# Kernel optimization log

Hardware: AMD Instinct MI355X
Metric: run time of the kernel (lower is better)

## Reference

```python
import jax, jax.numpy as jnp
import numpy as np

# ---- init_kwargs-derived constants ----
B, IN_F, OUT_F = 8192, 4096, 4096
W_SCALE = 0.01          # layer_params['w_scale']
B_SCALE = 0.01          # layer_params['b_scale']
IN_MIN, IN_MAX = -1.0, 1.0   # input_stats
NUM_BITS = 8
QMAX = 2 ** NUM_BITS - 1
IN_SCALE = (IN_MAX - IN_MIN) / QMAX
IN_ZP = int(round(-IN_MIN / (IN_SCALE + 1e-12)))


def setup_inputs() -> dict:
    key = jax.random.key(0)
    k1, k2, k3 = jax.random.split(key, 3)
    x_float = jax.random.normal(k1, (B, IN_F), dtype=jnp.float32)
    # int8-range weights/bias (stored as int32 containers)
    w_q = jax.random.randint(k2, (OUT_F, IN_F), -128, 128, dtype=jnp.int32)
    b_q = jax.random.randint(k3, (OUT_F,), -128, 128, dtype=jnp.int32)
    return {"x_float": x_float, "w_q": w_q, "b_q": b_q}


def reference(x_float, w_q, b_q):
    # quantize input to uint8 range [0,255]
    x_q = jnp.clip(jnp.round(x_float / IN_SCALE + IN_ZP), 0, 255).astype(jnp.int32)
    x_shifted = x_q - IN_ZP                       # [B, IN_F] int32
    # exact int32 accumulation matmul: [B, IN_F] @ [IN_F, OUT_F]
    acc_int = jnp.matmul(x_shifted, w_q.T, preferred_element_type=jnp.int32)
    out = acc_int.astype(jnp.float32) * (IN_SCALE * W_SCALE)
    out = out + b_q.astype(jnp.float32) * B_SCALE  # bias_float = b_q * b_scale
    return out
```

## Files before the change

### kernel.cpp

```cpp
#include <hip/hip_runtime.h>
#include <stdint.h>

constexpr int Mdim = 8192;
constexpr int Ndim = 4096;
constexpr int Kdim = 4096;
constexpr int NT = Kdim / 128;

#define ISF        ((float)(2.0 / 255.0))
#define OUT_SCALE  ((float)(2.0 / 255.0 * 0.01))
#define BSCALE     0.01f

typedef int i32x4 __attribute__((ext_vector_type(4)));

__global__ __launch_bounds__(256) void quantize_x(const float* __restrict__ x,
                                                  int* __restrict__ x8,
                                                  int ngroups) {
  int idx = blockIdx.x * 256 + threadIdx.x;
  int stride = gridDim.x * 256;
  for (int g = idx; g < ngroups; g += stride) {
    float4 v = reinterpret_cast<const float4*>(x)[g];
    int a0 = (int)rintf(v.x / ISF + 127.0f);
    int a1 = (int)rintf(v.y / ISF + 127.0f);
    int a2 = (int)rintf(v.z / ISF + 127.0f);
    int a3 = (int)rintf(v.w / ISF + 127.0f);
    a0 = a0 < 0 ? 0 : (a0 > 255 ? 255 : a0); a0 -= 128;
    a1 = a1 < 0 ? 0 : (a1 > 255 ? 255 : a1); a1 -= 128;
    a2 = a2 < 0 ? 0 : (a2 > 255 ? 255 : a2); a2 -= 128;
    a3 = a3 < 0 ? 0 : (a3 > 255 ? 255 : a3); a3 -= 128;
    x8[g] = (a0 & 0xff) | ((a1 & 0xff) << 8) | ((a2 & 0xff) << 16) |
            (int)(((unsigned)(a3 & 0xff)) << 24);
  }
}

__global__ __launch_bounds__(256) void convert_w(const int* __restrict__ wq,
                                                 int* __restrict__ w8,
                                                 int* __restrict__ wsum) {
  int row = blockIdx.x;
  const int4* src = reinterpret_cast<const int4*>(wq + (size_t)row * Kdim);
  int* dst = w8 + (size_t)row * (Kdim / 4);
  int s = 0;
#pragma unroll
  for (int i = 0; i < 4; ++i) {
    int idx = i * 256 + threadIdx.x;
    int4 v = src[idx];
    s += v.x + v.y + v.z + v.w;
    dst[idx] = (v.x & 0xff) | ((v.y & 0xff) << 8) | ((v.z & 0xff) << 16) |
               (int)(((unsigned)(v.w & 0xff)) << 24);
  }
  __shared__ int red[256];
  red[threadIdx.x] = s;
  __syncthreads();
  for (int off = 128; off; off >>= 1) {
    if ((int)threadIdx.x < off) red[threadIdx.x] += red[threadIdx.x + off];
    __syncthreads();
  }
  if (threadIdx.x == 0) wsum[row] = red[0];
}

#define AS1C const __attribute__((address_space(1))) void*
#define AS3  __attribute__((address_space(3))) void*
#define GLL(src, dst) __builtin_amdgcn_global_load_lds((AS1C)(src), (AS3)(dst), 16, 0, 0)
#define BAR() asm volatile("s_barrier" ::: "memory")
#define LGK0() do { asm volatile("s_waitcnt lgkmcnt(0)" ::: "memory"); \
                    __builtin_amdgcn_sched_barrier(0); } while (0)
#define VMC(N) asm volatile("s_waitcnt vmcnt(" #N ")" ::: "memory")
#define MFMA(a, b, c) __builtin_amdgcn_mfma_i32_16x16x64_i8(a, b, c, 0, 0, 0)
#define BBASE 98304

__global__ __launch_bounds__(512, 2) void gemm_i8_q(const int8_t* __restrict__ A8,
                                                    const int8_t* __restrict__ B8,
                                                    const int* __restrict__ wsum,
                                                    const int* __restrict__ bq,
                                                    float* __restrict__ out) {
  __shared__ uint8_t lds[163840];

  int bid = blockIdx.x;
  int wg = (bid & 7) * 64 + (bid >> 3);
  int bm = wg >> 4;
  int bn = wg & 15;

  const int tid = threadIdx.x;
  const int lane = tid & 63;
  const int wv = tid >> 6;
  const int wr = wv >> 2;
  const int wc = wv & 3;
  const int l15 = lane & 15, hi = lane >> 4;

  const int r3 = lane >> 3, s3 = lane & 7;
  const int swcol = (s3 ^ r3) << 4;
  const size_t aoff = (size_t)(bm * 256 + wv * 8 + r3) * Kdim + swcol;
  const size_t boff = (size_t)(bn * 256 + wv * 8 + r3) * Kdim + swcol;
  const int ldsw = wv * 1024;

#define ISSUE_A(P, t, half) do { \
    GLL(A8 + aoff + (size_t)(t) * 128 + (size_t)((half) * 128) * Kdim, \
        &lds[(P) * 32768 + (half) * 16384 + ldsw]); \
    GLL(A8 + aoff + (size_t)(t) * 128 + (size_t)((half) * 128 + 64) * Kdim, \
        &lds[(P) * 32768 + (half) * 16384 + 8192 + ldsw]); \
  } while (0)
#define ISSUE_B(P, t, half) do { \
    GLL(B8 + boff + (size_t)(t) * 128 + (size_t)((half) * 128) * Kdim, \
        &lds[BBASE + (P) * 32768 + (half) * 16384 + ldsw]); \
    GLL(B8 + boff + (size_t)(t) * 128 + (size_t)((half) * 128 + 64) * Kdim, \
        &lds[BBASE + (P) * 32768 + (half) * 16384 + 8192 + ldsw]); \
  } while (0)

  const int aRow = (wr * 128 + l15) * 128;
  const int bRow = (wc * 64 + l15) * 128;
  const int sl0 = (hi ^ (l15 & 7)) << 4;
  const int sl1 = ((4 + hi) ^ (l15 & 7)) << 4;

#define LDA(P, i, ks) (*reinterpret_cast<const i32x4*>( \
    &lds[(P) * 32768 + aRow + (i) * 2048 + ((ks) ? sl1 : sl0)]))
#define LDB(P, j, ks) (*reinterpret_cast<const i32x4*>( \
    &lds[BBASE + (P) * 32768 + bRow + (j) * 2048 + ((ks) ? sl1 : sl0)]))

  i32x4 acc[8][4];
#pragma unroll
  for (int i = 0; i < 8; ++i)
#pragma unroll
    for (int j = 0; j < 4; ++j) acc[i][j] = (i32x4){0, 0, 0, 0};

  ISSUE_A(0, 0, 0); ISSUE_A(0, 0, 1);
  ISSUE_B(0, 0, 0); ISSUE_B(0, 0, 1);
  ISSUE_A(1, 1, 0); ISSUE_A(1, 1, 1);
  VMC(4);
  BAR();

#define TILE(TA, TB, TA2, t, DOB, DOA, VM4, VM0) do { \
    i32x4 a_[4], B0[4], B1[4]; \
     \
    if (DOB) ISSUE_B((TB) ^ 1, (t) + 1, 0); \
    B0[0] = LDB(TB, 0, 0); B0[1] = LDB(TB, 1, 0); B0[2] = LDB(TB, 2, 0); B0[3] = LDB(TB, 3, 0); \
    a_[0] = LDA(TA, 0, 0); a_[1] = LDA(TA, 1, 0); a_[2] = LDA(TA, 2, 0); a_[3] = LDA(TA, 3, 0); \
    BAR(); LGK0(); __builtin_amdgcn_s_setprio(1); \
    _Pragma("unroll") for (int i = 0; i < 4; ++i) \
      _Pragma("unroll") for (int j = 0; j < 4; ++j) \
        acc[i][j] = MFMA(a_[i], B0[j], acc[i][j]); \
    __builtin_amdgcn_s_setprio(0); BAR(); \
     \
    if (DOB) ISSUE_B((TB) ^ 1, (t) + 1, 1); \
    a_[0] = LDA(TA, 4, 0); a_[1] = LDA(TA, 5, 0); a_[2] = LDA(TA, 6, 0); a_[3] = LDA(TA, 7, 0); \
    BAR(); LGK0(); __builtin_amdgcn_s_setprio(1); \
    _Pragma("unroll") for (int i = 0; i < 4; ++i) \
      _Pragma("unroll") for (int j = 0; j < 4; ++j) \
        acc[i + 4][j] = MFMA(a_[i], B0[j], acc[i + 4][j]); \
    __builtin_amdgcn_s_setprio(0); BAR(); \
     \
    if (DOA) ISSUE_A(TA2, (t) + 2, 0); \
    B1[0] = LDB(TB, 0, 1); B1[1] = LDB(TB, 1, 1); B1[2] = LDB(TB, 2, 1); B1[3] = LDB(TB, 3, 1); \
    a_[0] = LDA(TA, 0, 1); a_[1] = LDA(TA, 1, 1); a_[2] = LDA(TA, 2, 1); a_[3] = LDA(TA, 3, 1); \
    BAR(); LGK0(); __builtin_amdgcn_s_setprio(1); \
    _Pragma("unroll") for (int i = 0; i < 4; ++i) \
      _Pragma("unroll") for (int j = 0; j < 4; ++j) \
        acc[i][j] = MFMA(a_[i], B1[j], acc[i][j]); \
    __builtin_amdgcn_s_setprio(0); BAR(); \
     \
    if (DOA) ISSUE_A(TA2, (t) + 2, 1); \
    a_[0] = LDA(TA, 4, 1); a_[1] = LDA(TA, 5, 1); a_[2] = LDA(TA, 6, 1); a_[3] = LDA(TA, 7, 1); \
    BAR(); LGK0(); __builtin_amdgcn_s_setprio(1); \
    _Pragma("unroll") for (int i = 0; i < 4; ++i) \
      _Pragma("unroll") for (int j = 0; j < 4; ++j) \
        acc[i + 4][j] = MFMA(a_[i], B1[j], acc[i + 4][j]); \
    __builtin_amdgcn_s_setprio(0); \
    if (VM4) VMC(4); \
    if (VM0) VMC(0); \
    BAR(); \
  } while (0)

  for (int it = 0; it < 5; ++it) {
    int t = it * 6;
    TILE(0, 0, 2, t + 0, 1, 1, 1, 0);
    TILE(1, 1, 0, t + 1, 1, 1, 1, 0);
    TILE(2, 0, 1, t + 2, 1, 1, 1, 0);
    TILE(0, 1, 2, t + 3, 1, 1, 1, 0);
    TILE(1, 0, 0, t + 4, 1, 1, 1, 0);
    TILE(2, 1, 1, t + 5, 1, 1, 1, 0);
  }
  TILE(0, 0, 2, 30, 1, 0, 0, 1);
  TILE(1, 1, 0, 31, 0, 0, 0, 0);

#pragma unroll
  for (int j = 0; j < 4; ++j) {
    int col = bn * 256 + wc * 64 + j * 16 + l15;
    float fb = (float)bq[col] * BSCALE;
    int ws = wsum[col];
#pragma unroll
    for (int i = 0; i < 8; ++i) {
      int rbase = bm * 256 + wr * 128 + i * 16 + hi * 4;
#pragma unroll
      for (int p = 0; p < 4; ++p)
        out[(size_t)(rbase + p) * Ndim + col] = (float)(acc[i][j][p] + ws) * OUT_SCALE + fb;
    }
  }
#undef TILE
#undef ISSUE_A
#undef ISSUE_B
#undef LDA
#undef LDB
}

__global__ void fallback_kernel(const float* __restrict__ x, const int* __restrict__ wq,
                                const int* __restrict__ bq, float* __restrict__ out) {
  int col = blockIdx.x * 16 + (threadIdx.x & 15);
  int row = blockIdx.y * 16 + (threadIdx.x >> 4);
  const float* xr = x + (size_t)row * Kdim;
  const int* wr_ = wq + (size_t)col * Kdim;
  int acc = 0;
  for (int k = 0; k < Kdim; ++k) {
    int v = (int)rintf(xr[k] / ISF + 127.0f);
    v = v < 0 ? 0 : (v > 255 ? 255 : v);
    acc += (v - 127) * wr_[k];
  }
  out[(size_t)row * Ndim + col] = (float)acc * OUT_SCALE + (float)bq[col] * BSCALE;
}

extern "C" void kernel_launch(void* const* d_in, const int* in_sizes, int n_in,
                              void* d_out, int out_size, void* d_ws, size_t ws_size,
                              hipStream_t stream) {
  const float* x = (const float*)d_in[0];
  const int* wq = (const int*)d_in[1];
  const int* bq = (const int*)d_in[2];
  float* out = (float*)d_out;

  const size_t x8_bytes = (size_t)Mdim * Kdim;
  const size_t w8_bytes = (size_t)Ndim * Kdim;
  const size_t ws_need = x8_bytes + w8_bytes + (size_t)Ndim * sizeof(int);

  if (ws_size >= ws_need) {
    int8_t* x8 = (int8_t*)d_ws;
    int8_t* w8 = x8 + x8_bytes;
    int* wsum = (int*)(w8 + w8_bytes);

    quantize_x<<<2048, 256, 0, stream>>>(x, (int*)x8, Mdim * Kdim / 4);
    convert_w<<<Ndim, 256, 0, stream>>>(wq, (int*)w8, wsum);
    gemm_i8_q<<<(Mdim / 256) * (Ndim / 256), 512, 0, stream>>>(x8, w8, wsum, bq, out);
  } else {
    dim3 grid(Ndim / 16, Mdim / 16);
    fallback_kernel<<<grid, 256, 0, stream>>>(x, wq, bq, out);
  }
}
```

Baseline: 182.0 us.

## Software-pipeline LDS reads with partial lgkmcnt waits and fewer barriers

Restructures the per-tile schedule of the int8 GEMM. All global-to-LDS prefetches for the next tiles are issued at the start of each tile, and LDS fragment reads for later MFMA groups are issued ahead of the current group. Partial lgkmcnt waits replace the full waits and three of the four intra-tile s_barriers, so LDS latency overlaps with MFMA work. This raises register pressure (more live fragments) and relies on vmcnt/lgkmcnt counting being correct now that each tile has fewer barriers; issuing all prefetches early could race on LDS buffers if the triple-buffering is off.

```diff
diff --git a/kernel.cpp b/kernel.cpp
--- a/kernel.cpp
+++ b/kernel.cpp
@@ -61,17 +61,17 @@
 #define AS3  __attribute__((address_space(3))) void*
 #define GLL(src, dst) __builtin_amdgcn_global_load_lds((AS1C)(src), (AS3)(dst), 16, 0, 0)
 #define BAR() asm volatile("s_barrier" ::: "memory")
-#define LGK0() do { asm volatile("s_waitcnt lgkmcnt(0)" ::: "memory"); \
-                    __builtin_amdgcn_sched_barrier(0); } while (0)
+#define SB0() __builtin_amdgcn_sched_barrier(0)
+#define LGK(N) do { asm volatile("s_waitcnt lgkmcnt(" #N ")" ::: "memory"); SB0(); } while (0)
 #define VMC(N) asm volatile("s_waitcnt vmcnt(" #N ")" ::: "memory")
 #define MFMA(a, b, c) __builtin_amdgcn_mfma_i32_16x16x64_i8(a, b, c, 0, 0, 0)
 #define BBASE 98304
 
-__global__ __launch_bounds__(512, 2) void gemm_i8_q(const int8_t* __restrict__ A8,
-                                                    const int8_t* __restrict__ B8,
-                                                    const int* __restrict__ wsum,
-                                                    const int* __restrict__ bq,
-                                                    float* __restrict__ out) {
+__global__ __launch_bounds__(512, 2) void gemm_i8_pipe(const int8_t* __restrict__ A8,
+                                                       const int8_t* __restrict__ B8,
+                                                       const int* __restrict__ wsum,
+                                                       const int* __restrict__ bq,
+                                                       float* __restrict__ out) {
   __shared__ uint8_t lds[163840];
 
   int bid = blockIdx.x;
@@ -121,6 +121,12 @@
 #pragma unroll
     for (int j = 0; j < 4; ++j) acc[i][j] = (i32x4){0, 0, 0, 0};
 
+#define GRP(AV, BV, IOFF) do { \
+    _Pragma("unroll") for (int i = 0; i < 4; ++i) \
+      _Pragma("unroll") for (int j = 0; j < 4; ++j) \
+        acc[i + (IOFF)][j] = MFMA(AV[i], BV[j], acc[i + (IOFF)][j]); \
+  } while (0)
+
   ISSUE_A(0, 0, 0); ISSUE_A(0, 0, 1);
   ISSUE_B(0, 0, 0); ISSUE_B(0, 0, 1);
   ISSUE_A(1, 1, 0); ISSUE_A(1, 1, 1);
@@ -128,40 +134,38 @@
   BAR();
 
 #define TILE(TA, TB, TA2, t, DOB, DOA, VM4, VM0) do { \
-    i32x4 a_[4], B0[4], B1[4]; \
-     \
-    if (DOB) ISSUE_B((TB) ^ 1, (t) + 1, 0); \
+    if (DOB) { ISSUE_B((TB) ^ 1, (t) + 1, 0); ISSUE_B((TB) ^ 1, (t) + 1, 1); } \
+    if (DOA) { ISSUE_A(TA2, (t) + 2, 0); ISSUE_A(TA2, (t) + 2, 1); } \
+    i32x4 B0[4], B1[4], a0[4], a1[4], a2[4], a3[4]; \
+     \
     B0[0] = LDB(TB, 0, 0); B0[1] = LDB(TB, 1, 0); B0[2] = LDB(TB, 2, 0); B0[3] = LDB(TB, 3, 0); \
-    a_[0] = LDA(TA, 0, 0); a_[1] = LDA(TA, 1, 0); a_[2] = LDA(TA, 2, 0); a_[3] = LDA(TA, 3, 0); \
-    BAR(); LGK0(); __builtin_amdgcn_s_setprio(1); \
-    _Pragma("unroll") for (int i = 0; i < 4; ++i) \
-      _Pragma("unroll") for (int j = 0; j < 4; ++j) \
-        acc[i][j] = MFMA(a_[i], B0[j], acc[i][j]); \
-    __builtin_amdgcn_s_setprio(0); BAR(); \
-     \
-    if (DOB) ISSUE_B((TB) ^ 1, (t) + 1, 1); \
-    a_[0] = LDA(TA, 4, 0); a_[1] = LDA(TA, 5, 0); a_[2] = LDA(TA, 6, 0); a_[3] = LDA(TA, 7, 0); \
-    BAR(); LGK0(); __builtin_amdgcn_s_setprio(1); \
-    _Pragma("unroll") for (int i = 0; i < 4; ++i) \
-      _Pragma("unroll") for (int j = 0; j < 4; ++j) \
-        acc[i + 4][j] = MFMA(a_[i], B0[j], acc[i + 4][j]); \
-    __builtin_amdgcn_s_setprio(0); BAR(); \
-     \
-    if (DOA) ISSUE_A(TA2, (t) + 2, 0); \
+    a0[0] = LDA(TA, 0, 0); a0[1] = LDA(TA, 1, 0); a0[2] = LDA(TA, 2, 0); a0[3] = LDA(TA, 3, 0); \
+    SB0(); \
+     \
+    a1[0] = LDA(TA, 4, 0); a1[1] = LDA(TA, 5, 0); a1[2] = LDA(TA, 6, 0); a1[3] = LDA(TA, 7, 0); \
     B1[0] = LDB(TB, 0, 1); B1[1] = LDB(TB, 1, 1); B1[2] = LDB(TB, 2, 1); B1[3] = LDB(TB, 3, 1); \
-    a_[0] = LDA(TA, 0, 1); a_[1] = LDA(TA, 1, 1); a_[2] = LDA(TA, 2, 1); a_[3] = LDA(TA, 3, 1); \
-    BAR(); LGK0(); __builtin_amdgcn_s_setprio(1); \
-    _Pragma("unroll") for (int i = 0; i < 4; ++i) \
-      _Pragma("unroll") for (int j = 0; j < 4; ++j) \
-        acc[i][j] = MFMA(a_[i], B1[j], acc[i][j]); \
-    __builtin_amdgcn_s_setprio(0); BAR(); \
-     \
-    if (DOA) ISSUE_A(TA2, (t) + 2, 1); \
-    a_[0] = LDA(TA, 4, 1); a_[1] = LDA(TA, 5, 1); a_[2] = LDA(TA, 6, 1); a_[3] = LDA(TA, 7, 1); \
-    BAR(); LGK0(); __builtin_amdgcn_s_setprio(1); \
-    _Pragma("unroll") for (int i = 0; i < 4; ++i) \
-      _Pragma("unroll") for (int j = 0; j < 4; ++j) \
-        acc[i + 4][j] = MFMA(a_[i], B1[j], acc[i + 4][j]); \
+    SB0(); \
+    LGK(8);   \
+    __builtin_amdgcn_s_setprio(1); \
+    GRP(a0, B0, 0); \
+    __builtin_amdgcn_s_setprio(0); SB0(); \
+     \
+    a2[0] = LDA(TA, 0, 1); a2[1] = LDA(TA, 1, 1); a2[2] = LDA(TA, 2, 1); a2[3] = LDA(TA, 3, 1); \
+    SB0(); \
+    LGK(4);   \
+    __builtin_amdgcn_s_setprio(1); \
+    GRP(a1, B0, 4); \
+    __builtin_amdgcn_s_setprio(0); SB0(); \
+     \
+    a3[0] = LDA(TA, 4, 1); a3[1] = LDA(TA, 5, 1); a3[2] = LDA(TA, 6, 1); a3[3] = LDA(TA, 7, 1); \
+    SB0(); \
+    LGK(4);   \
+    __builtin_amdgcn_s_setprio(1); \
+    GRP(a2, B1, 0); \
+    __builtin_amdgcn_s_setprio(0); SB0(); \
+    LGK(0);   \
+    __builtin_amdgcn_s_setprio(1); \
+    GRP(a3, B1, 4); \
     __builtin_amdgcn_s_setprio(0); \
     if (VM4) VMC(4); \
     if (VM0) VMC(0); \
@@ -194,6 +198,7 @@
     }
   }
 #undef TILE
+#undef GRP
 #undef ISSUE_A
 #undef ISSUE_B
 #undef LDA
@@ -234,7 +239,7 @@
 
     quantize_x<<<2048, 256, 0, stream>>>(x, (int*)x8, Mdim * Kdim / 4);
     convert_w<<<Ndim, 256, 0, stream>>>(wq, (int*)w8, wsum);
-    gemm_i8_q<<<(Mdim / 256) * (Ndim / 256), 512, 0, stream>>>(x8, w8, wsum, bq, out);
+    gemm_i8_pipe<<<(Mdim / 256) * (Ndim / 256), 512, 0, stream>>>(x8, w8, wsum, bq, out);
   } else {
     dim3 grid(Ndim / 16, Mdim / 16);
     fallback_kernel<<<grid, 256, 0, stream>>>(x, wq, bq, out);
```

Result: no change. 180.1 us (-1.1%).

## Drop intra-tile barriers and let compiler schedule LDS reads and MFMAs

Applied to the files above, without the earlier changes.

Each K-tile loses its three intermediate workgroup barriers, the explicit lgkmcnt waits with sched_barrier, and the setprio toggles, keeping only the final barrier. All four global-to-LDS prefetches for the tile are now issued at the start rather than spread across the four phases. All eight A fragments per k-slice are loaded into registers before running the 8x4 MFMA block. This aims to cut barrier stalls and let the compiler overlap LDS reads with MFMAs, at the cost of more live vector registers and less explicit control over issue order.

```diff
diff --git a/kernel.cpp b/kernel.cpp
--- a/kernel.cpp
+++ b/kernel.cpp
@@ -61,17 +61,15 @@
 #define AS3  __attribute__((address_space(3))) void*
 #define GLL(src, dst) __builtin_amdgcn_global_load_lds((AS1C)(src), (AS3)(dst), 16, 0, 0)
 #define BAR() asm volatile("s_barrier" ::: "memory")
-#define LGK0() do { asm volatile("s_waitcnt lgkmcnt(0)" ::: "memory"); \
-                    __builtin_amdgcn_sched_barrier(0); } while (0)
 #define VMC(N) asm volatile("s_waitcnt vmcnt(" #N ")" ::: "memory")
 #define MFMA(a, b, c) __builtin_amdgcn_mfma_i32_16x16x64_i8(a, b, c, 0, 0, 0)
 #define BBASE 98304
 
-__global__ __launch_bounds__(512, 2) void gemm_i8_q(const int8_t* __restrict__ A8,
-                                                    const int8_t* __restrict__ B8,
-                                                    const int* __restrict__ wsum,
-                                                    const int* __restrict__ bq,
-                                                    float* __restrict__ out) {
+__global__ __launch_bounds__(512, 2) void gemm_i8_free(const int8_t* __restrict__ A8,
+                                                       const int8_t* __restrict__ B8,
+                                                       const int* __restrict__ wsum,
+                                                       const int* __restrict__ bq,
+                                                       float* __restrict__ out) {
   __shared__ uint8_t lds[163840];
 
   int bid = blockIdx.x;
@@ -128,41 +126,19 @@
   BAR();
 
 #define TILE(TA, TB, TA2, t, DOB, DOA, VM4, VM0) do { \
-    i32x4 a_[4], B0[4], B1[4]; \
-     \
-    if (DOB) ISSUE_B((TB) ^ 1, (t) + 1, 0); \
+    if (DOB) { ISSUE_B((TB) ^ 1, (t) + 1, 0); ISSUE_B((TB) ^ 1, (t) + 1, 1); } \
+    if (DOA) { ISSUE_A(TA2, (t) + 2, 0); ISSUE_A(TA2, (t) + 2, 1); } \
+    i32x4 a0[8], B0[4], a1[8], B1[4]; \
     B0[0] = LDB(TB, 0, 0); B0[1] = LDB(TB, 1, 0); B0[2] = LDB(TB, 2, 0); B0[3] = LDB(TB, 3, 0); \
-    a_[0] = LDA(TA, 0, 0); a_[1] = LDA(TA, 1, 0); a_[2] = LDA(TA, 2, 0); a_[3] = LDA(TA, 3, 0); \
-    BAR(); LGK0(); __builtin_amdgcn_s_setprio(1); \
-    _Pragma("unroll") for (int i = 0; i < 4; ++i) \
+    _Pragma("unroll") for (int i = 0; i < 8; ++i) a0[i] = LDA(TA, i, 0); \
+    _Pragma("unroll") for (int i = 0; i < 8; ++i) \
       _Pragma("unroll") for (int j = 0; j < 4; ++j) \
-        acc[i][j] = MFMA(a_[i], B0[j], acc[i][j]); \
-    __builtin_amdgcn_s_setprio(0); BAR(); \
-     \
-    if (DOB) ISSUE_B((TB) ^ 1, (t) + 1, 1); \
-    a_[0] = LDA(TA, 4, 0); a_[1] = LDA(TA, 5, 0); a_[2] = LDA(TA, 6, 0); a_[3] = LDA(TA, 7, 0); \
-    BAR(); LGK0(); __builtin_amdgcn_s_setprio(1); \
-    _Pragma("unroll") for (int i = 0; i < 4; ++i) \
+        acc[i][j] = MFMA(a0[i], B0[j], acc[i][j]); \
+    B1[0] = LDB(TB, 0, 1); B1[1] = LDB(TB, 1, 1); B1[2] = LDB(TB, 2, 1); B1[3] = LDB(TB, 3, 1); \
+    _Pragma("unroll") for (int i = 0; i < 8; ++i) a1[i] = LDA(TA, i, 1); \
+    _Pragma("unroll") for (int i = 0; i < 8; ++i) \
       _Pragma("unroll") for (int j = 0; j < 4; ++j) \
-        acc[i + 4][j] = MFMA(a_[i], B0[j], acc[i + 4][j]); \
-    __builtin_amdgcn_s_setprio(0); BAR(); \
-     \
-    if (DOA) ISSUE_A(TA2, (t) + 2, 0); \
-    B1[0] = LDB(TB, 0, 1); B1[1] = LDB(TB, 1, 1); B1[2] = LDB(TB, 2, 1); B1[3] = LDB(TB, 3, 1); \
-    a_[0] = LDA(TA, 0, 1); a_[1] = LDA(TA, 1, 1); a_[2] = LDA(TA, 2, 1); a_[3] = LDA(TA, 3, 1); \
-    BAR(); LGK0(); __builtin_amdgcn_s_setprio(1); \
-    _Pragma("unroll") for (int i = 0; i < 4; ++i) \
-      _Pragma("unroll") for (int j = 0; j < 4; ++j) \
-        acc[i][j] = MFMA(a_[i], B1[j], acc[i][j]); \
-    __builtin_amdgcn_s_setprio(0); BAR(); \
-     \
-    if (DOA) ISSUE_A(TA2, (t) + 2, 1); \
-    a_[0] = LDA(TA, 4, 1); a_[1] = LDA(TA, 5, 1); a_[2] = LDA(TA, 6, 1); a_[3] = LDA(TA, 7, 1); \
-    BAR(); LGK0(); __builtin_amdgcn_s_setprio(1); \
-    _Pragma("unroll") for (int i = 0; i < 4; ++i) \
-      _Pragma("unroll") for (int j = 0; j < 4; ++j) \
-        acc[i + 4][j] = MFMA(a_[i], B1[j], acc[i + 4][j]); \
-    __builtin_amdgcn_s_setprio(0); \
+        acc[i][j] = MFMA(a1[i], B1[j], acc[i][j]); \
     if (VM4) VMC(4); \
     if (VM0) VMC(0); \
     BAR(); \
@@ -234,7 +210,7 @@
 
     quantize_x<<<2048, 256, 0, stream>>>(x, (int*)x8, Mdim * Kdim / 4);
     convert_w<<<Ndim, 256, 0, stream>>>(wq, (int*)w8, wsum);
-    gemm_i8_q<<<(Mdim / 256) * (Ndim / 256), 512, 0, stream>>>(x8, w8, wsum, bq, out);
+    gemm_i8_free<<<(Mdim / 256) * (Ndim / 256), 512, 0, stream>>>(x8, w8, wsum, bq, out);
   } else {
     dim3 grid(Ndim / 16, Mdim / 16);
     fallback_kernel<<<grid, 256, 0, stream>>>(x, wq, bq, out);
```

After: 262.0 us. 1.44x slower.
